# Kernel tuning notes

Measured on AMD Instinct MI355X. Metric: run time of the kernel, lower is better.

The kernel has to match this reference:

```python
import jax, jax.numpy as jnp
import numpy as np

EPS = 1e-8  # torch F.cosine_similarity eps


def setup_inputs() -> dict:
    key = jax.random.key(0)
    k1, k2 = jax.random.split(key)
    z = jax.random.normal(k1, (32768, 2048), dtype=jnp.float32)
    expert_keys = jax.random.normal(k2, (64, 2048), dtype=jnp.float32)
    return {"z": z, "expert_keys": expert_keys}


def reference(z, expert_keys):
    # cosine similarity: (z . ek) / max(||z||*||ek||, eps)  -> [N, E]
    dots = jnp.einsum("nd,ed->ne", z, expert_keys)
    z_norm = jnp.linalg.norm(z, axis=-1)            # [N]
    e_norm = jnp.linalg.norm(expert_keys, axis=-1)  # [E]
    similarity = dots / jnp.maximum(z_norm[:, None] * e_norm[None, :], EPS)
    # softmax over experts, then weighted combination of expert keys -> [N, D]
    weighted_expert = jax.nn.softmax(similarity, axis=-1) @ expert_keys
    return similarity, weighted_expert
```

## Files before the change

### kernel.cpp

```cpp
#include <hip/hip_runtime.h>
#include <hip/hip_bf16.h>

typedef __attribute__((ext_vector_type(4))) float f32x4;
typedef __attribute__((ext_vector_type(8))) short bf16x8;

#define NROWS 32768
#define DIM   2048
#define NEXP  64

__device__ __forceinline__ short f2bf(float f) {
    __hip_bfloat16 h = __float2bfloat16(f);
    short s;
    __builtin_memcpy(&s, &h, 2);
    return s;
}

__global__ __launch_bounds__(256) void prep_experts(
    const float* __restrict__ ek,
    short* __restrict__ ekbf,
    short* __restrict__ ekT,
    float* __restrict__ enorm)
{
    const int e = blockIdx.x;
    const int t = threadIdx.x;
    const float* row = ek + e * DIM;
    float ss = 0.f;
#pragma unroll
    for (int i = 0; i < 2; ++i) {
        const int c4 = t + i * 256;
        const float4 v = ((const float4*)row)[c4];
        ss += v.x * v.x + v.y * v.y + v.z * v.z + v.w * v.w;
        short4 b;
        b.x = f2bf(v.x); b.y = f2bf(v.y); b.z = f2bf(v.z); b.w = f2bf(v.w);
        *(short4*)(ekbf + e * DIM + c4 * 4) = b;
        const int d = c4 * 4;
        ekT[(d + 0) * NEXP + e] = b.x;
        ekT[(d + 1) * NEXP + e] = b.y;
        ekT[(d + 2) * NEXP + e] = b.z;
        ekT[(d + 3) * NEXP + e] = b.w;
    }
#pragma unroll
    for (int s = 1; s < 64; s <<= 1) ss += __shfl_xor(ss, s);
    __shared__ float red[4];
    if ((t & 63) == 0) red[t >> 6] = ss;
    __syncthreads();
    if (t == 0) enorm[e] = sqrtf(red[0] + red[1] + red[2] + red[3]);
}

__global__ __launch_bounds__(256) void cosmoe_main(
    const float* __restrict__ z,
    const short* __restrict__ ekbf,
    const short* __restrict__ ekT,
    const float* __restrict__ enorm,
    float* __restrict__ out_sim,
    float* __restrict__ out_wei)
{
    const int tid = threadIdx.x;
    const int w   = tid >> 6;
    const int l   = tid & 63;
    const int lr  = l & 15;
    const int lg  = l >> 4;
    const int base_row = blockIdx.x * 64;

    const float* zrow = z + (size_t)(base_row + w * 16 + lr) * DIM + lg * 8;
    f32x4 acc[4];
#pragma unroll
    for (int nt = 0; nt < 4; ++nt) acc[nt] = f32x4{0.f, 0.f, 0.f, 0.f};
    float ssq = 0.f;

    for (int kk = 0; kk < DIM / 32; ++kk) {
        const float4 a0 = *(const float4*)(zrow + kk * 32);
        const float4 a1 = *(const float4*)(zrow + kk * 32 + 4);
        ssq += a0.x * a0.x + a0.y * a0.y + a0.z * a0.z + a0.w * a0.w
             + a1.x * a1.x + a1.y * a1.y + a1.z * a1.z + a1.w * a1.w;
        bf16x8 af;
        af[0] = f2bf(a0.x); af[1] = f2bf(a0.y); af[2] = f2bf(a0.z); af[3] = f2bf(a0.w);
        af[4] = f2bf(a1.x); af[5] = f2bf(a1.y); af[6] = f2bf(a1.z); af[7] = f2bf(a1.w);
        const int koff = kk * 32 + lg * 8;
#pragma unroll
        for (int nt = 0; nt < 4; ++nt) {
            const bf16x8 bf = *(const bf16x8*)(ekbf + (nt * 16 + lr) * DIM + koff);
            acc[nt] = __builtin_amdgcn_mfma_f32_16x16x32_bf16(af, bf, acc[nt], 0, 0, 0);
        }
    }
    ssq += __shfl_xor(ssq, 16);
    ssq += __shfl_xor(ssq, 32);
    const float zn_mine = sqrtf(ssq);

    float zn_j[4];
#pragma unroll
    for (int j = 0; j < 4; ++j) zn_j[j] = __shfl(zn_mine, lg * 4 + j);
    float en_nt[4];
#pragma unroll
    for (int nt = 0; nt < 4; ++nt) en_nt[nt] = enorm[nt * 16 + lr];

    float sim[4][4];
#pragma unroll
    for (int j = 0; j < 4; ++j)
#pragma unroll
        for (int nt = 0; nt < 4; ++nt)
            sim[nt][j] = acc[nt][j] / fmaxf(zn_j[j] * en_nt[nt], 1e-8f);

#pragma unroll
    for (int j = 0; j < 4; ++j) {
        const size_t ro = (size_t)(base_row + w * 16 + lg * 4 + j) * NEXP + lr;
#pragma unroll
        for (int nt = 0; nt < 4; ++nt) out_sim[ro + nt * 16] = sim[nt][j];
    }

    float wgt[4][4];
#pragma unroll
    for (int j = 0; j < 4; ++j) {
        float mx = fmaxf(fmaxf(sim[0][j], sim[1][j]), fmaxf(sim[2][j], sim[3][j]));
#pragma unroll
        for (int s = 1; s < 16; s <<= 1) mx = fmaxf(mx, __shfl_xor(mx, s));
        float sum = 0.f;
#pragma unroll
        for (int nt = 0; nt < 4; ++nt) { wgt[nt][j] = __expf(sim[nt][j] - mx); sum += wgt[nt][j]; }
#pragma unroll
        for (int s = 1; s < 16; s <<= 1) sum += __shfl_xor(sum, s);
        const float inv = 1.0f / sum;
#pragma unroll
        for (int nt = 0; nt < 4; ++nt) wgt[nt][j] *= inv;
    }

    __shared__ __align__(16) short Wl[4][16][72];
#pragma unroll
    for (int j = 0; j < 4; ++j)
#pragma unroll
        for (int nt = 0; nt < 4; ++nt)
            Wl[w][lg * 4 + j][nt * 16 + lr] = f2bf(wgt[nt][j]);
    __syncthreads();

    bf16x8 afr[4][2];
#pragma unroll
    for (int mt = 0; mt < 4; ++mt)
#pragma unroll
        for (int ks = 0; ks < 2; ++ks)
            afr[mt][ks] = *(const bf16x8*)&Wl[mt][lr][ks * 32 + lg * 8];

    for (int ntl = 0; ntl < 32; ++ntl) {
        const int d0 = w * 512 + ntl * 16;
        const short* bp = ekT + (size_t)(d0 + lr) * NEXP + lg * 8;
        const bf16x8 b0 = *(const bf16x8*)bp;
        const bf16x8 b1 = *(const bf16x8*)(bp + 32);
        f32x4 oacc[4];
#pragma unroll
        for (int mt = 0; mt < 4; ++mt) {
            oacc[mt] = f32x4{0.f, 0.f, 0.f, 0.f};
            oacc[mt] = __builtin_amdgcn_mfma_f32_16x16x32_bf16(afr[mt][0], b0, oacc[mt], 0, 0, 0);
            oacc[mt] = __builtin_amdgcn_mfma_f32_16x16x32_bf16(afr[mt][1], b1, oacc[mt], 0, 0, 0);
        }
#pragma unroll
        for (int mt = 0; mt < 4; ++mt)
#pragma unroll
            for (int j = 0; j < 4; ++j)
                out_wei[(size_t)(base_row + mt * 16 + lg * 4 + j) * DIM + d0 + lr] = oacc[mt][j];
    }
}

extern "C" void kernel_launch(void* const* d_in, const int* in_sizes, int n_in,
                              void* d_out, int out_size, void* d_ws, size_t ws_size,
                              hipStream_t stream) {
    const float* z  = (const float*)d_in[0];
    const float* ek = (const float*)d_in[1];
    float* out_sim = (float*)d_out;
    float* out_wei = out_sim + (size_t)NROWS * NEXP;

    short* ekbf  = (short*)d_ws;
    short* ekT   = ekbf + NEXP * DIM;
    float* enorm = (float*)(ekT + DIM * NEXP);

    prep_experts<<<NEXP, 256, 0, stream>>>(ek, ekbf, ekT, enorm);
    cosmoe_main<<<NROWS / 64, 256, 0, stream>>>(z, ekbf, ekT, enorm, out_sim, out_wei);
}
```

Before: 162.2 us.

## Split K across wave pairs and halve rows per block to double grid

```diff
diff --git a/kernel.cpp b/kernel.cpp
--- a/kernel.cpp
+++ b/kernel.cpp
@@ -60,99 +60,133 @@
     const int l   = tid & 63;
     const int lr  = l & 15;
     const int lg  = l >> 4;
-    const int base_row = blockIdx.x * 64;
-
-    const float* zrow = z + (size_t)(base_row + w * 16 + lr) * DIM + lg * 8;
+    const int p   = w >> 1;
+    const int s   = w & 1;
+    const int base_row = blockIdx.x * 32;
+
+    __shared__ float racc[2][64][17];
+    __shared__ float rssq[2][16];
+    __shared__ __align__(16) short Wl[2][16][72];
+
+    const float* zrow = z + (size_t)(base_row + p * 16 + lr) * DIM + s * 1024 + lg * 8;
     f32x4 acc[4];
 #pragma unroll
     for (int nt = 0; nt < 4; ++nt) acc[nt] = f32x4{0.f, 0.f, 0.f, 0.f};
-    float ssq = 0.f;
-
-    for (int kk = 0; kk < DIM / 32; ++kk) {
-        const float4 a0 = *(const float4*)(zrow + kk * 32);
-        const float4 a1 = *(const float4*)(zrow + kk * 32 + 4);
-        ssq += a0.x * a0.x + a0.y * a0.y + a0.z * a0.z + a0.w * a0.w
-             + a1.x * a1.x + a1.y * a1.y + a1.z * a1.z + a1.w * a1.w;
-        bf16x8 af;
-        af[0] = f2bf(a0.x); af[1] = f2bf(a0.y); af[2] = f2bf(a0.z); af[3] = f2bf(a0.w);
-        af[4] = f2bf(a1.x); af[5] = f2bf(a1.y); af[6] = f2bf(a1.z); af[7] = f2bf(a1.w);
-        const int koff = kk * 32 + lg * 8;
-#pragma unroll
-        for (int nt = 0; nt < 4; ++nt) {
-            const bf16x8 bf = *(const bf16x8*)(ekbf + (nt * 16 + lr) * DIM + koff);
-            acc[nt] = __builtin_amdgcn_mfma_f32_16x16x32_bf16(af, bf, acc[nt], 0, 0, 0);
-        }
-    }
+    float ss0 = 0.f, ss1 = 0.f, ss2 = 0.f, ss3 = 0.f;
+
+    for (int kk = 0; kk < 32; kk += 4) {
+        float4 v[8];
+#pragma unroll
+        for (int u = 0; u < 4; ++u) {
+            v[2 * u]     = *(const float4*)(zrow + (kk + u) * 32);
+            v[2 * u + 1] = *(const float4*)(zrow + (kk + u) * 32 + 4);
+        }
+#pragma unroll
+        for (int u = 0; u < 4; ++u) {
+            const float4 a0 = v[2 * u], a1 = v[2 * u + 1];
+            ss0 = fmaf(a0.x, a0.x, ss0); ss1 = fmaf(a0.y, a0.y, ss1);
+            ss2 = fmaf(a0.z, a0.z, ss2); ss3 = fmaf(a0.w, a0.w, ss3);
+            ss0 = fmaf(a1.x, a1.x, ss0); ss1 = fmaf(a1.y, a1.y, ss1);
+            ss2 = fmaf(a1.z, a1.z, ss2); ss3 = fmaf(a1.w, a1.w, ss3);
+            bf16x8 af;
+            af[0] = f2bf(a0.x); af[1] = f2bf(a0.y); af[2] = f2bf(a0.z); af[3] = f2bf(a0.w);
+            af[4] = f2bf(a1.x); af[5] = f2bf(a1.y); af[6] = f2bf(a1.z); af[7] = f2bf(a1.w);
+            const int koff = s * 1024 + (kk + u) * 32 + lg * 8;
+#pragma unroll
+            for (int nt = 0; nt < 4; ++nt) {
+                const bf16x8 bf = *(const bf16x8*)(ekbf + (nt * 16 + lr) * DIM + koff);
+                acc[nt] = __builtin_amdgcn_mfma_f32_16x16x32_bf16(af, bf, acc[nt], 0, 0, 0);
+            }
+        }
+    }
+    float ssq = (ss0 + ss1) + (ss2 + ss3);
     ssq += __shfl_xor(ssq, 16);
     ssq += __shfl_xor(ssq, 32);
-    const float zn_mine = sqrtf(ssq);
-
-    float zn_j[4];
-#pragma unroll
-    for (int j = 0; j < 4; ++j) zn_j[j] = __shfl(zn_mine, lg * 4 + j);
-    float en_nt[4];
-#pragma unroll
-    for (int nt = 0; nt < 4; ++nt) en_nt[nt] = enorm[nt * 16 + lr];
-
-    float sim[4][4];
-#pragma unroll
-    for (int j = 0; j < 4; ++j)
+
+    if (s == 1) {
 #pragma unroll
         for (int nt = 0; nt < 4; ++nt)
-            sim[nt][j] = acc[nt][j] / fmaxf(zn_j[j] * en_nt[nt], 1e-8f);
-
-#pragma unroll
-    for (int j = 0; j < 4; ++j) {
-        const size_t ro = (size_t)(base_row + w * 16 + lg * 4 + j) * NEXP + lr;
-#pragma unroll
-        for (int nt = 0; nt < 4; ++nt) out_sim[ro + nt * 16] = sim[nt][j];
-    }
-
-    float wgt[4][4];
-#pragma unroll
-    for (int j = 0; j < 4; ++j) {
-        float mx = fmaxf(fmaxf(sim[0][j], sim[1][j]), fmaxf(sim[2][j], sim[3][j]));
-#pragma unroll
-        for (int s = 1; s < 16; s <<= 1) mx = fmaxf(mx, __shfl_xor(mx, s));
-        float sum = 0.f;
-#pragma unroll
-        for (int nt = 0; nt < 4; ++nt) { wgt[nt][j] = __expf(sim[nt][j] - mx); sum += wgt[nt][j]; }
-#pragma unroll
-        for (int s = 1; s < 16; s <<= 1) sum += __shfl_xor(sum, s);
-        const float inv = 1.0f / sum;
-#pragma unroll
-        for (int nt = 0; nt < 4; ++nt) wgt[nt][j] *= inv;
-    }
-
-    __shared__ __align__(16) short Wl[4][16][72];
-#pragma unroll
-    for (int j = 0; j < 4; ++j)
+#pragma unroll
+            for (int j = 0; j < 4; ++j) racc[p][l][nt * 4 + j] = acc[nt][j];
+        if (l < 16) rssq[p][l] = ssq;
+    }
+    __syncthreads();
+
+    if (s == 0) {
 #pragma unroll
         for (int nt = 0; nt < 4; ++nt)
-            Wl[w][lg * 4 + j][nt * 16 + lr] = f2bf(wgt[nt][j]);
+#pragma unroll
+            for (int j = 0; j < 4; ++j) acc[nt][j] += racc[p][l][nt * 4 + j];
+        ssq += rssq[p][lr];
+        const float zn_mine = sqrtf(ssq);
+
+        float zn_j[4];
+#pragma unroll
+        for (int j = 0; j < 4; ++j) zn_j[j] = __shfl(zn_mine, lg * 4 + j);
+        float en_nt[4];
+#pragma unroll
+        for (int nt = 0; nt < 4; ++nt) en_nt[nt] = enorm[nt * 16 + lr];
+
+        float sim[4][4];
+#pragma unroll
+        for (int j = 0; j < 4; ++j)
+#pragma unroll
+            for (int nt = 0; nt < 4; ++nt)
+                sim[nt][j] = acc[nt][j] / fmaxf(zn_j[j] * en_nt[nt], 1e-8f);
+
+#pragma unroll
+        for (int j = 0; j < 4; ++j) {
+            const size_t ro = (size_t)(base_row + p * 16 + lg * 4 + j) * NEXP + lr;
+#pragma unroll
+            for (int nt = 0; nt < 4; ++nt) out_sim[ro + nt * 16] = sim[nt][j];
+        }
+
+        float wgt[4][4];
+#pragma unroll
+        for (int j = 0; j < 4; ++j) {
+            float mx = fmaxf(fmaxf(sim[0][j], sim[1][j]), fmaxf(sim[2][j], sim[3][j]));
+#pragma unroll
+            for (int t = 1; t < 16; t <<= 1) mx = fmaxf(mx, __shfl_xor(mx, t));
+            float sum = 0.f;
+#pragma unroll
+            for (int nt = 0; nt < 4; ++nt) { wgt[nt][j] = __expf(sim[nt][j] - mx); sum += wgt[nt][j]; }
+#pragma unroll
+            for (int t = 1; t < 16; t <<= 1) sum += __shfl_xor(sum, t);
+            const float inv = 1.0f / sum;
+#pragma unroll
+            for (int nt = 0; nt < 4; ++nt) wgt[nt][j] *= inv;
+        }
+
+#pragma unroll
+        for (int j = 0; j < 4; ++j)
+#pragma unroll
+            for (int nt = 0; nt < 4; ++nt)
+                Wl[p][lg * 4 + j][nt * 16 + lr] = f2bf(wgt[nt][j]);
+    }
     __syncthreads();
 
-    bf16x8 afr[4][2];
-#pragma unroll
-    for (int mt = 0; mt < 4; ++mt)
+    bf16x8 afr[2][2];
+#pragma unroll
+    for (int mt = 0; mt < 2; ++mt)
 #pragma unroll
         for (int ks = 0; ks < 2; ++ks)
             afr[mt][ks] = *(const bf16x8*)&Wl[mt][lr][ks * 32 + lg * 8];
 
+#pragma unroll 2
     for (int ntl = 0; ntl < 32; ++ntl) {
         const int d0 = w * 512 + ntl * 16;
         const short* bp = ekT + (size_t)(d0 + lr) * NEXP + lg * 8;
         const bf16x8 b0 = *(const bf16x8*)bp;
         const bf16x8 b1 = *(const bf16x8*)(bp + 32);
-        f32x4 oacc[4];
-#pragma unroll
-        for (int mt = 0; mt < 4; ++mt) {
+        f32x4 oacc[2];
+#pragma unroll
+        for (int mt = 0; mt < 2; ++mt) {
             oacc[mt] = f32x4{0.f, 0.f, 0.f, 0.f};
             oacc[mt] = __builtin_amdgcn_mfma_f32_16x16x32_bf16(afr[mt][0], b0, oacc[mt], 0, 0, 0);
             oacc[mt] = __builtin_amdgcn_mfma_f32_16x16x32_bf16(afr[mt][1], b1, oacc[mt], 0, 0, 0);
         }
 #pragma unroll
-        for (int mt = 0; mt < 4; ++mt)
+        for (int mt = 0; mt < 2; ++mt)
 #pragma unroll
             for (int j = 0; j < 4; ++j)
                 out_wei[(size_t)(base_row + mt * 16 + lg * 4 + j) * DIM + d0 + lr] = oacc[mt][j];
@@ -172,5 +206,5 @@
     float* enorm = (float*)(ekT + DIM * NEXP);
 
     prep_experts<<<NEXP, 256, 0, stream>>>(ek, ekbf, ekT, enorm);
-    cosmoe_main<<<NROWS / 64, 256, 0, stream>>>(z, ekbf, ekT, enorm, out_sim, out_wei);
-}
+    cosmoe_main<<<NROWS / 32, 256, 0, stream>>>(z, ekbf, ekT, enorm, out_sim, out_wei);
+}
```

Measured after the change: 187.5 us. 15.5% more time.

## Software-pipeline global loads in both GEMM phases and use nontemporal output stores

Applied to the files above, without the earlier changes.

```diff
diff --git a/kernel.cpp b/kernel.cpp
--- a/kernel.cpp
+++ b/kernel.cpp
@@ -47,7 +47,47 @@
     if (t == 0) enorm[e] = sqrtf(red[0] + red[1] + red[2] + red[3]);
 }
 
-__global__ __launch_bounds__(256) void cosmoe_main(
+
+struct P1Buf { float4 z0, z1; bf16x8 e0, e1, e2, e3; };
+
+__device__ __forceinline__ void p1_load(P1Buf& b, const float* zrow,
+                                        const short* ekbf, int lr, int lg, int kk) {
+    b.z0 = *(const float4*)(zrow + kk * 32);
+    b.z1 = *(const float4*)(zrow + kk * 32 + 4);
+    const int koff = kk * 32 + lg * 8;
+    b.e0 = *(const bf16x8*)(ekbf + (0 * 16 + lr) * DIM + koff);
+    b.e1 = *(const bf16x8*)(ekbf + (1 * 16 + lr) * DIM + koff);
+    b.e2 = *(const bf16x8*)(ekbf + (2 * 16 + lr) * DIM + koff);
+    b.e3 = *(const bf16x8*)(ekbf + (3 * 16 + lr) * DIM + koff);
+}
+
+__device__ __forceinline__ void p1_compute(const P1Buf& b, f32x4 acc[4],
+        float& s0, float& s1, float& s2, float& s3) {
+    const float4 a0 = b.z0, a1 = b.z1;
+    s0 = fmaf(a0.x, a0.x, s0); s1 = fmaf(a0.y, a0.y, s1);
+    s2 = fmaf(a0.z, a0.z, s2); s3 = fmaf(a0.w, a0.w, s3);
+    s0 = fmaf(a1.x, a1.x, s0); s1 = fmaf(a1.y, a1.y, s1);
+    s2 = fmaf(a1.z, a1.z, s2); s3 = fmaf(a1.w, a1.w, s3);
+    bf16x8 af;
+    af[0] = f2bf(a0.x); af[1] = f2bf(a0.y); af[2] = f2bf(a0.z); af[3] = f2bf(a0.w);
+    af[4] = f2bf(a1.x); af[5] = f2bf(a1.y); af[6] = f2bf(a1.z); af[7] = f2bf(a1.w);
+    acc[0] = __builtin_amdgcn_mfma_f32_16x16x32_bf16(af, b.e0, acc[0], 0, 0, 0);
+    acc[1] = __builtin_amdgcn_mfma_f32_16x16x32_bf16(af, b.e1, acc[1], 0, 0, 0);
+    acc[2] = __builtin_amdgcn_mfma_f32_16x16x32_bf16(af, b.e2, acc[2], 0, 0, 0);
+    acc[3] = __builtin_amdgcn_mfma_f32_16x16x32_bf16(af, b.e3, acc[3], 0, 0, 0);
+}
+
+struct P3Buf { bf16x8 b0, b1; };
+
+__device__ __forceinline__ void p3_load(P3Buf& b, const short* ekT,
+                                        int w, int lr, int lg, int ntl) {
+    const int d0 = w * 512 + ntl * 16;
+    const short* bp = ekT + (size_t)(d0 + lr) * NEXP + lg * 8;
+    b.b0 = *(const bf16x8*)bp;
+    b.b1 = *(const bf16x8*)(bp + 32);
+}
+
+__global__ __launch_bounds__(256, 2) void cosmoe_main(
     const float* __restrict__ z,
     const short* __restrict__ ekbf,
     const short* __restrict__ ekT,
@@ -66,23 +106,26 @@
     f32x4 acc[4];
 #pragma unroll
     for (int nt = 0; nt < 4; ++nt) acc[nt] = f32x4{0.f, 0.f, 0.f, 0.f};
-    float ssq = 0.f;
-
-    for (int kk = 0; kk < DIM / 32; ++kk) {
-        const float4 a0 = *(const float4*)(zrow + kk * 32);
-        const float4 a1 = *(const float4*)(zrow + kk * 32 + 4);
-        ssq += a0.x * a0.x + a0.y * a0.y + a0.z * a0.z + a0.w * a0.w
-             + a1.x * a1.x + a1.y * a1.y + a1.z * a1.z + a1.w * a1.w;
-        bf16x8 af;
-        af[0] = f2bf(a0.x); af[1] = f2bf(a0.y); af[2] = f2bf(a0.z); af[3] = f2bf(a0.w);
-        af[4] = f2bf(a1.x); af[5] = f2bf(a1.y); af[6] = f2bf(a1.z); af[7] = f2bf(a1.w);
-        const int koff = kk * 32 + lg * 8;
-#pragma unroll
-        for (int nt = 0; nt < 4; ++nt) {
-            const bf16x8 bf = *(const bf16x8*)(ekbf + (nt * 16 + lr) * DIM + koff);
-            acc[nt] = __builtin_amdgcn_mfma_f32_16x16x32_bf16(af, bf, acc[nt], 0, 0, 0);
-        }
-    }
+    float ss0 = 0.f, ss1 = 0.f, ss2 = 0.f, ss3 = 0.f;
+
+    P1Buf A, B, C, D;
+    p1_load(A, zrow, ekbf, lr, lg, 0);
+    p1_load(B, zrow, ekbf, lr, lg, 1);
+    p1_load(C, zrow, ekbf, lr, lg, 2);
+    p1_load(D, zrow, ekbf, lr, lg, 3);
+
+    for (int kk = 0; kk < 64; kk += 4) {
+        p1_compute(A, acc, ss0, ss1, ss2, ss3);
+        if (kk < 60) p1_load(A, zrow, ekbf, lr, lg, kk + 4);
+        p1_compute(B, acc, ss0, ss1, ss2, ss3);
+        if (kk < 60) p1_load(B, zrow, ekbf, lr, lg, kk + 5);
+        p1_compute(C, acc, ss0, ss1, ss2, ss3);
+        if (kk < 60) p1_load(C, zrow, ekbf, lr, lg, kk + 6);
+        p1_compute(D, acc, ss0, ss1, ss2, ss3);
+        if (kk < 60) p1_load(D, zrow, ekbf, lr, lg, kk + 7);
+    }
+
+    float ssq = (ss0 + ss1) + (ss2 + ss3);
     ssq += __shfl_xor(ssq, 16);
     ssq += __shfl_xor(ssq, 32);
     const float zn_mine = sqrtf(ssq);
@@ -105,7 +148,8 @@
     for (int j = 0; j < 4; ++j) {
         const size_t ro = (size_t)(base_row + w * 16 + lg * 4 + j) * NEXP + lr;
 #pragma unroll
-        for (int nt = 0; nt < 4; ++nt) out_sim[ro + nt * 16] = sim[nt][j];
+        for (int nt = 0; nt < 4; ++nt)
+            __builtin_nontemporal_store(sim[nt][j], &out_sim[ro + nt * 16]);
     }
 
     float wgt[4][4];
@@ -113,12 +157,12 @@
     for (int j = 0; j < 4; ++j) {
         float mx = fmaxf(fmaxf(sim[0][j], sim[1][j]), fmaxf(sim[2][j], sim[3][j]));
 #pragma unroll
-        for (int s = 1; s < 16; s <<= 1) mx = fmaxf(mx, __shfl_xor(mx, s));
+        for (int t = 1; t < 16; t <<= 1) mx = fmaxf(mx, __shfl_xor(mx, t));
         float sum = 0.f;
 #pragma unroll
         for (int nt = 0; nt < 4; ++nt) { wgt[nt][j] = __expf(sim[nt][j] - mx); sum += wgt[nt][j]; }
 #pragma unroll
-        for (int s = 1; s < 16; s <<= 1) sum += __shfl_xor(sum, s);
+        for (int t = 1; t < 16; t <<= 1) sum += __shfl_xor(sum, t);
         const float inv = 1.0f / sum;
 #pragma unroll
         for (int nt = 0; nt < 4; ++nt) wgt[nt][j] *= inv;
@@ -139,23 +183,45 @@
         for (int ks = 0; ks < 2; ++ks)
             afr[mt][ks] = *(const bf16x8*)&Wl[mt][lr][ks * 32 + lg * 8];
 
-    for (int ntl = 0; ntl < 32; ++ntl) {
-        const int d0 = w * 512 + ntl * 16;
-        const short* bp = ekT + (size_t)(d0 + lr) * NEXP + lg * 8;
-        const bf16x8 b0 = *(const bf16x8*)bp;
-        const bf16x8 b1 = *(const bf16x8*)(bp + 32);
-        f32x4 oacc[4];
-#pragma unroll
-        for (int mt = 0; mt < 4; ++mt) {
-            oacc[mt] = f32x4{0.f, 0.f, 0.f, 0.f};
-            oacc[mt] = __builtin_amdgcn_mfma_f32_16x16x32_bf16(afr[mt][0], b0, oacc[mt], 0, 0, 0);
-            oacc[mt] = __builtin_amdgcn_mfma_f32_16x16x32_bf16(afr[mt][1], b1, oacc[mt], 0, 0, 0);
+    P3Buf PA, PB;
+    p3_load(PA, ekT, w, lr, lg, 0);
+    p3_load(PB, ekT, w, lr, lg, 1);
+
+    for (int base = 0; base < 32; base += 2) {
+        {
+            const int d0 = w * 512 + base * 16;
+            f32x4 oacc[4];
+#pragma unroll
+            for (int mt = 0; mt < 4; ++mt) {
+                oacc[mt] = f32x4{0.f, 0.f, 0.f, 0.f};
+                oacc[mt] = __builtin_amdgcn_mfma_f32_16x16x32_bf16(afr[mt][0], PA.b0, oacc[mt], 0, 0, 0);
+                oacc[mt] = __builtin_amdgcn_mfma_f32_16x16x32_bf16(afr[mt][1], PA.b1, oacc[mt], 0, 0, 0);
+            }
+            if (base < 30) p3_load(PA, ekT, w, lr, lg, base + 2);
+#pragma unroll
+            for (int mt = 0; mt < 4; ++mt)
+#pragma unroll
+                for (int j = 0; j < 4; ++j)
+                    __builtin_nontemporal_store(oacc[mt][j],
+                        &out_wei[(size_t)(base_row + mt * 16 + lg * 4 + j) * DIM + d0 + lr]);
         }
-#pragma unroll
-        for (int mt = 0; mt < 4; ++mt)
-#pragma unroll
-            for (int j = 0; j < 4; ++j)
-                out_wei[(size_t)(base_row + mt * 16 + lg * 4 + j) * DIM + d0 + lr] = oacc[mt][j];
+        {
+            const int d0 = w * 512 + (base + 1) * 16;
+            f32x4 oacc[4];
+#pragma unroll
+            for (int mt = 0; mt < 4; ++mt) {
+                oacc[mt] = f32x4{0.f, 0.f, 0.f, 0.f};
+                oacc[mt] = __builtin_amdgcn_mfma_f32_16x16x32_bf16(afr[mt][0], PB.b0, oacc[mt], 0, 0, 0);
+                oacc[mt] = __builtin_amdgcn_mfma_f32_16x16x32_bf16(afr[mt][1], PB.b1, oacc[mt], 0, 0, 0);
+            }
+            if (base < 30) p3_load(PB, ekT, w, lr, lg, base + 3);
+#pragma unroll
+            for (int mt = 0; mt < 4; ++mt)
+#pragma unroll
+                for (int j = 0; j < 4; ++j)
+                    __builtin_nontemporal_store(oacc[mt][j],
+                        &out_wei[(size_t)(base_row + mt * 16 + lg * 4 + j) * DIM + d0 + lr]);
+        }
     }
 }
 
```

Measured after the change: 177.2 us. +9.2%, slower.

## Stage z and expert tiles through LDS with async multi-buffered loads

Applied to the files above, without the earlier changes.

```diff
diff --git a/kernel.cpp b/kernel.cpp
--- a/kernel.cpp
+++ b/kernel.cpp
@@ -7,12 +7,19 @@
 #define NROWS 32768
 #define DIM   2048
 #define NEXP  64
+#define NC    64
 
 __device__ __forceinline__ short f2bf(float f) {
     __hip_bfloat16 h = __float2bfloat16(f);
     short s;
     __builtin_memcpy(&s, &h, 2);
     return s;
+}
+
+__device__ __forceinline__ void async16(const void* g, void* l) {
+    __builtin_amdgcn_global_load_lds(
+        (const __attribute__((address_space(1))) unsigned int*)g,
+        (__attribute__((address_space(3))) unsigned int*)l, 16, 0, 0);
 }
 
 __global__ __launch_bounds__(256) void prep_experts(
@@ -45,6 +52,17 @@
     if ((t & 63) == 0) red[t >> 6] = ss;
     __syncthreads();
     if (t == 0) enorm[e] = sqrtf(red[0] + red[1] + red[2] + red[3]);
+}
+
+
+struct P3Buf { bf16x8 b0, b1; };
+
+__device__ __forceinline__ void p3_load(P3Buf& b, const short* ekT,
+                                        int w, int lr, int lg, int ntl) {
+    const int d0 = w * 512 + ntl * 16;
+    const short* bp = ekT + (size_t)(d0 + lr) * NEXP + lg * 8;
+    b.b0 = *(const bf16x8*)bp;
+    b.b1 = *(const bf16x8*)(bp + 32);
 }
 
 __global__ __launch_bounds__(256) void cosmoe_main(
@@ -62,27 +80,58 @@
     const int lg  = l >> 4;
     const int base_row = blockIdx.x * 64;
 
-    const float* zrow = z + (size_t)(base_row + w * 16 + lr) * DIM + lg * 8;
+    __shared__ __align__(16) float zbuf[4][64][32];
+    __shared__ __align__(16) short ebuf[4][64][32];
+    __shared__ __align__(16) short Wl[4][16][72];
+
+    const int zcolu = ((l & 7) ^ (l >> 3));
+    const float* zg0 = z + (size_t)(base_row + w * 16 + (l >> 3)) * DIM + zcolu * 4;
+    const float* zg1 = z + (size_t)(base_row + w * 16 + 8 + (l >> 3)) * DIM + zcolu * 4;
+    const int ecolu = ((l & 3) ^ ((l >> 2) & 3));
+    const short* eg = ekbf + (size_t)(w * 16 + (l >> 2)) * DIM + ecolu * 8;
+
+#define STAGE(c_) do { const int b_ = (c_) & 3;                     \
+        async16(zg0 + (size_t)(c_) * 32, &zbuf[b_][w * 16][0]);     \
+        async16(zg1 + (size_t)(c_) * 32, &zbuf[b_][w * 16 + 8][0]); \
+        async16(eg  + (c_) * 32,         &ebuf[b_][w * 16][0]);     \
+    } while (0)
+
     f32x4 acc[4];
 #pragma unroll
     for (int nt = 0; nt < 4; ++nt) acc[nt] = f32x4{0.f, 0.f, 0.f, 0.f};
-    float ssq = 0.f;
-
-    for (int kk = 0; kk < DIM / 32; ++kk) {
-        const float4 a0 = *(const float4*)(zrow + kk * 32);
-        const float4 a1 = *(const float4*)(zrow + kk * 32 + 4);
-        ssq += a0.x * a0.x + a0.y * a0.y + a0.z * a0.z + a0.w * a0.w
-             + a1.x * a1.x + a1.y * a1.y + a1.z * a1.z + a1.w * a1.w;
+    float ss0 = 0.f, ss1 = 0.f;
+
+    STAGE(0); STAGE(1); STAGE(2);
+
+    for (int c = 0; c < NC; ++c) {
+        if (c < NC - 2)       asm volatile("s_waitcnt vmcnt(6)" ::: "memory");
+        else if (c == NC - 2) asm volatile("s_waitcnt vmcnt(3)" ::: "memory");
+        else                  asm volatile("s_waitcnt vmcnt(0)" ::: "memory");
+        __builtin_amdgcn_s_barrier();
+        __builtin_amdgcn_sched_barrier(0);
+        if (c < NC - 3) STAGE(c + 3);
+
+        const int b = c & 3;
+        const char* zrowp = (const char*)&zbuf[b][w * 16 + lr][0];
+        const float4 a0 = *(const float4*)(zrowp + ((((lg * 2)    ) ^ (lr & 7)) << 4));
+        const float4 a1 = *(const float4*)(zrowp + ((((lg * 2) + 1) ^ (lr & 7)) << 4));
+        ss0 = fmaf(a0.x, a0.x, ss0); ss1 = fmaf(a0.y, a0.y, ss1);
+        ss0 = fmaf(a0.z, a0.z, ss0); ss1 = fmaf(a0.w, a0.w, ss1);
+        ss0 = fmaf(a1.x, a1.x, ss0); ss1 = fmaf(a1.y, a1.y, ss1);
+        ss0 = fmaf(a1.z, a1.z, ss0); ss1 = fmaf(a1.w, a1.w, ss1);
         bf16x8 af;
         af[0] = f2bf(a0.x); af[1] = f2bf(a0.y); af[2] = f2bf(a0.z); af[3] = f2bf(a0.w);
         af[4] = f2bf(a1.x); af[5] = f2bf(a1.y); af[6] = f2bf(a1.z); af[7] = f2bf(a1.w);
-        const int koff = kk * 32 + lg * 8;
+        const int se = (lg ^ (lr & 3)) << 4;
 #pragma unroll
         for (int nt = 0; nt < 4; ++nt) {
-            const bf16x8 bf = *(const bf16x8*)(ekbf + (nt * 16 + lr) * DIM + koff);
+            const bf16x8 bf = *(const bf16x8*)((const char*)&ebuf[b][nt * 16 + lr][0] + se);
             acc[nt] = __builtin_amdgcn_mfma_f32_16x16x32_bf16(af, bf, acc[nt], 0, 0, 0);
         }
     }
+#undef STAGE
+
+    float ssq = ss0 + ss1;
     ssq += __shfl_xor(ssq, 16);
     ssq += __shfl_xor(ssq, 32);
     const float zn_mine = sqrtf(ssq);
@@ -113,18 +162,17 @@
     for (int j = 0; j < 4; ++j) {
         float mx = fmaxf(fmaxf(sim[0][j], sim[1][j]), fmaxf(sim[2][j], sim[3][j]));
 #pragma unroll
-        for (int s = 1; s < 16; s <<= 1) mx = fmaxf(mx, __shfl_xor(mx, s));
+        for (int t = 1; t < 16; t <<= 1) mx = fmaxf(mx, __shfl_xor(mx, t));
         float sum = 0.f;
 #pragma unroll
         for (int nt = 0; nt < 4; ++nt) { wgt[nt][j] = __expf(sim[nt][j] - mx); sum += wgt[nt][j]; }
 #pragma unroll
-        for (int s = 1; s < 16; s <<= 1) sum += __shfl_xor(sum, s);
+        for (int t = 1; t < 16; t <<= 1) sum += __shfl_xor(sum, t);
         const float inv = 1.0f / sum;
 #pragma unroll
         for (int nt = 0; nt < 4; ++nt) wgt[nt][j] *= inv;
     }
 
-    __shared__ __align__(16) short Wl[4][16][72];
 #pragma unroll
     for (int j = 0; j < 4; ++j)
 #pragma unroll
@@ -139,23 +187,43 @@
         for (int ks = 0; ks < 2; ++ks)
             afr[mt][ks] = *(const bf16x8*)&Wl[mt][lr][ks * 32 + lg * 8];
 
-    for (int ntl = 0; ntl < 32; ++ntl) {
-        const int d0 = w * 512 + ntl * 16;
-        const short* bp = ekT + (size_t)(d0 + lr) * NEXP + lg * 8;
-        const bf16x8 b0 = *(const bf16x8*)bp;
-        const bf16x8 b1 = *(const bf16x8*)(bp + 32);
-        f32x4 oacc[4];
-#pragma unroll
-        for (int mt = 0; mt < 4; ++mt) {
-            oacc[mt] = f32x4{0.f, 0.f, 0.f, 0.f};
-            oacc[mt] = __builtin_amdgcn_mfma_f32_16x16x32_bf16(afr[mt][0], b0, oacc[mt], 0, 0, 0);
-            oacc[mt] = __builtin_amdgcn_mfma_f32_16x16x32_bf16(afr[mt][1], b1, oacc[mt], 0, 0, 0);
+    P3Buf PA, PB;
+    p3_load(PA, ekT, w, lr, lg, 0);
+    p3_load(PB, ekT, w, lr, lg, 1);
+
+    for (int base = 0; base < 32; base += 2) {
+        {
+            const int d0 = w * 512 + base * 16;
+            f32x4 oacc[4];
+#pragma unroll
+            for (int mt = 0; mt < 4; ++mt) {
+                oacc[mt] = f32x4{0.f, 0.f, 0.f, 0.f};
+                oacc[mt] = __builtin_amdgcn_mfma_f32_16x16x32_bf16(afr[mt][0], PA.b0, oacc[mt], 0, 0, 0);
+                oacc[mt] = __builtin_amdgcn_mfma_f32_16x16x32_bf16(afr[mt][1], PA.b1, oacc[mt], 0, 0, 0);
+            }
+            if (base < 30) p3_load(PA, ekT, w, lr, lg, base + 2);
+#pragma unroll
+            for (int mt = 0; mt < 4; ++mt)
+#pragma unroll
+                for (int j = 0; j < 4; ++j)
+                    out_wei[(size_t)(base_row + mt * 16 + lg * 4 + j) * DIM + d0 + lr] = oacc[mt][j];
         }
-#pragma unroll
-        for (int mt = 0; mt < 4; ++mt)
-#pragma unroll
-            for (int j = 0; j < 4; ++j)
-                out_wei[(size_t)(base_row + mt * 16 + lg * 4 + j) * DIM + d0 + lr] = oacc[mt][j];
+        {
+            const int d0 = w * 512 + (base + 1) * 16;
+            f32x4 oacc[4];
+#pragma unroll
+            for (int mt = 0; mt < 4; ++mt) {
+                oacc[mt] = f32x4{0.f, 0.f, 0.f, 0.f};
+                oacc[mt] = __builtin_amdgcn_mfma_f32_16x16x32_bf16(afr[mt][0], PB.b0, oacc[mt], 0, 0, 0);
+                oacc[mt] = __builtin_amdgcn_mfma_f32_16x16x32_bf16(afr[mt][1], PB.b1, oacc[mt], 0, 0, 0);
+            }
+            if (base < 30) p3_load(PB, ekT, w, lr, lg, base + 3);
+#pragma unroll
+            for (int mt = 0; mt < 4; ++mt)
+#pragma unroll
+                for (int j = 0; j < 4; ++j)
+                    out_wei[(size_t)(base_row + mt * 16 + lg * 4 + j) * DIM + d0 + lr] = oacc[mt][j];
+        }
     }
 }
 
```

After: 181.1 us. 1.12x slower.
